# Kernel tuning notes

Measured on AMD Instinct MI355X. Metric: run time of the kernel, lower is better.

The kernel has to match this reference:

```python
import jax, jax.numpy as jnp
import numpy as np

B, T, D, H, E, O, A = 8192, 223, 7, 128, 50, 29, 9
IMPUTE_W, LABEL_W = 0.3, 1.0

def setup_inputs() -> dict:
    key = jax.random.key(0)
    ks = jax.random.split(key, 32)
    u = lambda k, shape, fan: jax.random.uniform(k, shape, jnp.float32, -1.0/np.sqrt(fan), 1.0/np.sqrt(fan))
    return {
        'values':    jax.random.normal(ks[0], (B, T, D), jnp.float32),
        'masks':     (jax.random.uniform(ks[1], (B, T, D)) < 0.8).astype(jnp.float32),
        'deltas':    jax.random.uniform(ks[2], (B, T, D), jnp.float32) * 5.0,
        'probs':     jax.nn.softmax(jax.random.normal(ks[3], (B, O), jnp.float32), axis=1),
        'ancillary': jax.random.normal(ks[4], (B, A), jnp.float32),
        'labels':    jax.random.randint(ks[5], (B,), 0, O, jnp.int32),
        'W_td_h': u(ks[6], (H, D), H),  'b_td_h': u(ks[7], (H,), H),
        'W_td_x': u(ks[8], (D, D), D),  'b_td_x': u(ks[9], (D,), D),
        'W_hist': u(ks[10], (D, H), H), 'b_hist': u(ks[11], (D,), H),
        'W_feat': u(ks[12], (D, D), D), 'b_feat': u(ks[13], (D,), D),
        'W_comb': u(ks[14], (D, 2*D), 2*D), 'b_comb': u(ks[15], (D,), 2*D),
        'W_ih': u(ks[16], (4*H, 2*D), H), 'W_hh': u(ks[17], (4*H, H), H),
        'b_ih': u(ks[18], (4*H,), H),     'b_hh': u(ks[19], (4*H,), H),
        'W_anc': u(ks[20], (E, A), A),    'b_anc': u(ks[21], (E,), A),
        'W_cat': u(ks[22], (H, H + E), H + E), 'b_cat': u(ks[23], (H,), H + E),
        'W_out': u(ks[24], (O, H), H),    'b_out': u(ks[25], (O,), H),
    }

def _rits_forward(values, masks, deltas, probs, ancillary,
                  W_td_h, b_td_h, W_td_x, b_td_x, W_hist, b_hist,
                  W_feat, b_feat, W_comb, b_comb, W_ih, W_hh, b_ih, b_hh,
                  W_anc, b_anc, W_cat, b_cat, W_out, b_out):
    Bn = values.shape[0]
    td_x_diag = jnp.diag(W_td_x)                     # diag=True decay uses only diagonal
    Wf = W_feat * (1.0 - jnp.eye(D, dtype=W_feat.dtype))

    def step(carry, xt):
        h, c, xl = carry
        x, m, d = xt                                  # each [B, D]
        gamma_h = jnp.exp(-jax.nn.relu(d @ W_td_h.T + b_td_h))   # [B, H]
        gamma_x = jnp.exp(-jax.nn.relu(d * td_x_diag + b_td_x))  # [B, D]
        h = h * gamma_h
        x_h = h @ W_hist.T + b_hist
        msum = jnp.sum(m) + 1e-5
        xl = xl + jnp.sum(jnp.abs(x - x_h) * m) / msum
        x_c = m * x + (1.0 - m) * x_h
        z_h = x_c @ Wf.T + b_feat
        xl = xl + jnp.sum(jnp.abs(x - z_h) * m) / msum
        alpha = jnp.concatenate([gamma_x, m], axis=1) @ W_comb.T + b_comb
        c_h = alpha * z_h + (1.0 - alpha) * x_h
        xl = xl + jnp.sum(jnp.abs(x - c_h) * m) / msum
        c_c = m * x + (1.0 - m) * c_h
        inputs = jnp.concatenate([c_c, m], axis=1)    # [B, 2D]
        gates = inputs @ W_ih.T + b_ih + h @ W_hh.T + b_hh  # [B, 4H]
        i, f, g, o = jnp.split(gates, 4, axis=1)
        c = jax.nn.sigmoid(f) * c + jax.nn.sigmoid(i) * jnp.tanh(g)
        h = jax.nn.sigmoid(o) * jnp.tanh(c)
        return (h, c, xl), c_c

    h0 = jnp.zeros((Bn, H), values.dtype)
    c0 = jnp.zeros((Bn, H), values.dtype)
    xs = (jnp.swapaxes(values, 0, 1), jnp.swapaxes(masks, 0, 1), jnp.swapaxes(deltas, 0, 1))
    (h, c, x_loss), imps = jax.lax.scan(step, (h0, c0, jnp.float32(0.0)), xs)
    imputations = jnp.swapaxes(imps, 0, 1)           # [B, T, D]

    x_loss = x_loss * IMPUTE_W
    anc = jax.nn.relu(ancillary @ W_anc.T + b_anc)
    h = jax.nn.relu(jnp.concatenate([h, anc], axis=1) @ W_cat.T + b_cat)
    y_h = jax.nn.softmax(h @ W_out.T + b_out, axis=1)
    y_loss = jnp.sum((y_h - probs) ** 2) / (Bn + 1e-5) * LABEL_W
    return x_loss, y_loss, x_loss + y_loss, y_h, imputations

def reference(values, masks, deltas, probs, ancillary, labels,
              W_td_h, b_td_h, W_td_x, b_td_x, W_hist, b_hist,
              W_feat, b_feat, W_comb, b_comb, W_ih, W_hh, b_ih, b_hh,
              W_anc, b_anc, W_cat, b_cat, W_out, b_out):
    x_loss, y_loss, loss, y_h, imputations = _rits_forward(
        values, masks, deltas, probs, ancillary,
        W_td_h, b_td_h, W_td_x, b_td_x, W_hist, b_hist,
        W_feat, b_feat, W_comb, b_comb, W_ih, W_hh, b_ih, b_hh,
        W_anc, b_anc, W_cat, b_cat, W_out, b_out)
    return (x_loss, y_loss, loss, y_h, imputations, labels)
```

## Files before the change

kernel.cpp:

```cpp
#include <hip/hip_runtime.h>
#include <math.h>

#define B_ 8192
#define T_ 223
#define D_ 7
#define H_ 128
#define G_ 512
#define E_ 50
#define O_ 29
#define A_ 9
#define TD_ (T_*D_)
#define NB 32
#define NTHR 512
#define MB 8

#define WS_MINV  0
#define WS_ACC   (WS_MINV + T_)
#define WS_WCATT (WS_ACC + 2)
#define WS_HFIN  (WS_WCATT + 178*H_)

#define OUT_YH  3
#define OUT_IMP (OUT_YH + B_*O_)
#define OUT_LAB (OUT_IMP + B_*T_*D_)

typedef __attribute__((ext_vector_type(8))) short short8;
typedef __attribute__((ext_vector_type(4))) float floatx4;
#define MFMA16(Av,Bv,Cv) __builtin_amdgcn_mfma_f32_16x16x32_bf16((Av),(Bv),(Cv),0,0,0)

__device__ __forceinline__ unsigned short f2bf(float f) {
    unsigned int u = __builtin_bit_cast(unsigned int, f);
    return (unsigned short)((u + 0x7FFFu + ((u >> 16) & 1u)) >> 16);
}
__device__ __forceinline__ float bf2f(unsigned short s) {
    unsigned int u = ((unsigned int)s) << 16;
    return __builtin_bit_cast(float, u);
}
__device__ __forceinline__ float rcp_(float x)  { return __builtin_amdgcn_rcpf(x); }
__device__ __forceinline__ float sigm(float x)  { return rcp_(1.f + __expf(-x)); }
__device__ __forceinline__ float tanh_(float x) { return 1.f - 2.f*rcp_(1.f + __expf(2.f*x)); }

__global__ void rits_prep(const float* __restrict__ W_cat, float* __restrict__ ws)
{
    int idx = blockIdx.x * 256 + threadIdx.x;
    if (idx < H_*178) {
        int j = idx / 178, k = idx - j*178;
        ws[WS_WCATT + k*H_ + j] = W_cat[idx];
    }
    if (idx < 2) ws[WS_ACC + idx] = 0.f;
}

__global__ void rits_msum(const float* __restrict__ masks, float* __restrict__ ws)
{
    const int t = blockIdx.x, tid = threadIdx.x;
    float s = 0.f;
    for (int i = tid; i < B_*D_; i += 256) {
        int b = i / D_, q = i - b*D_;
        s += masks[b*TD_ + t*D_ + q];
    }
    for (int off = 32; off > 0; off >>= 1) s += __shfl_down(s, off, 64);
    __shared__ float r[4];
    if ((tid & 63) == 0) r[tid >> 6] = s;
    __syncthreads();
    if (tid == 0) ws[WS_MINV + t] = 1.f / (r[0]+r[1]+r[2]+r[3] + 1e-5f);
}

__global__ __launch_bounds__(NTHR, 2) void rits_main(
    const float* __restrict__ values, const float* __restrict__ masks, const float* __restrict__ deltas,
    const float* __restrict__ W_td_h, const float* __restrict__ b_td_h,
    const float* __restrict__ W_td_x, const float* __restrict__ b_td_x,
    const float* __restrict__ W_hist, const float* __restrict__ b_hist,
    const float* __restrict__ W_feat, const float* __restrict__ b_feat,
    const float* __restrict__ W_comb, const float* __restrict__ b_comb,
    const float* __restrict__ W_ih, const float* __restrict__ W_hh,
    const float* __restrict__ b_ih, const float* __restrict__ b_hh,
    float* __restrict__ ws, float* __restrict__ out)
{
    __shared__ __attribute__((aligned(16))) unsigned short hbuf[NB*168];
    __shared__ __attribute__((aligned(16))) unsigned short dbuf[NB*72];
    __shared__ __attribute__((aligned(16))) unsigned short whis_lds[16*136];
    __shared__ float xs[NB*8], msh[NB*8], dsl[NB*8];
    __shared__ float xh_l[NB*8], xc_l[NB*8], gx_l[NB*8];
    __shared__ float bhist_l[8], tdx_l[8], btdx_l[8];
    __shared__ float impbuf[NB*16*7];
    __shared__ float red[8];

    const int tid  = threadIdx.x;
    const int b0   = blockIdx.x * NB;
    const int lane = tid & 63;
    const int w    = tid >> 6;
    const int quad = lane >> 4;
    const int l15  = lane & 15;

    for (int i = tid; i < NB*168; i += NTHR) hbuf[i] = 0;
    for (int i = tid; i < NB*72;  i += NTHR) dbuf[i] = 0;
    for (int i = tid; i < 16*136; i += NTHR) {
        int r = i / 136, c = i - r*136;
        whis_lds[i] = (r < 7 && c < 128) ? f2bf(W_hist[r*H_ + c]) : 0;
    }
    if (tid < 8) {
        bhist_l[tid] = (tid < 7) ? b_hist[tid] : 0.f;
        tdx_l[tid]   = (tid < 7) ? W_td_x[tid*D_ + tid] : 0.f;
        btdx_l[tid]  = (tid < 7) ? b_td_x[tid] : 0.f;
    }

    short8 whhf[4][4];
    short8 winf[4];
    short8 wtdf;
    float  biasg_r[4][4];
    float  btdh_r[4];
    {
        union UU { short8 v; unsigned short u[8]; } fr;
        #pragma unroll
        for (int c = 0; c < 4; ++c) {
            const int j = (c*8 + w)*16 + l15;
            #pragma unroll
            for (int s = 0; s < 4; ++s) {
                const float* p = W_hh + j*H_ + s*32 + quad*8;
                #pragma unroll
                for (int e = 0; e < 8; ++e) fr.u[e] = f2bf(p[e]);
                whhf[c][s] = fr.v;
            }
            #pragma unroll
            for (int e = 0; e < 8; ++e) {
                int k = quad*8 + e;
                fr.u[e] = (k < 14) ? f2bf(W_ih[j*14 + k]) : (unsigned short)0;
            }
            winf[c] = fr.v;
            #pragma unroll
            for (int r = 0; r < 4; ++r) {
                int jj = (c*8 + w)*16 + quad*4 + r;
                biasg_r[c][r] = b_ih[jj] + b_hh[jj];
            }
        }
        #pragma unroll
        for (int e = 0; e < 8; ++e) {
            int k = quad*8 + e;
            fr.u[e] = (k < 7) ? f2bf(W_td_h[(w*16 + l15)*D_ + k]) : (unsigned short)0;
        }
        wtdf = fr.v;
        #pragma unroll
        for (int r = 0; r < 4; ++r) btdh_r[r] = b_td_h[w*16 + quad*4 + r];
    }

    const bool ldr = (tid < NB*D_);
    const int  lb  = tid / D_, li = tid - (tid/D_)*D_;
    float wfr[7], wcr[14], bfr = 0.f, bcr = 0.f;
    if (ldr) {
        #pragma unroll
        for (int k = 0; k < 7; ++k)  wfr[k] = (k == li) ? 0.f : W_feat[li*D_ + k];
        #pragma unroll
        for (int k = 0; k < 14; ++k) wcr[k] = W_comb[li*14 + k];
        bfr = b_feat[li];  bcr = b_comb[li];
    }

    float c_st[2][4] = {{0,0,0,0},{0,0,0,0}};
    float lacc = 0.f;

    const long gbase = (long)(b0 + lb)*TD_ + li;
    float rx = 0.f, rm = 0.f, rd = 0.f;
    if (ldr) { rx = values[gbase]; rm = masks[gbase]; rd = deltas[gbase]; }

    const float* minv = ws + WS_MINV;

    for (int t = 0; t < T_; ++t) {
        if (ldr) { xs[lb*8+li] = rx; msh[lb*8+li] = rm; dsl[lb*8+li] = rd; }
        __syncthreads();
        if (ldr && t + 1 < T_) {
            const long g = gbase + (long)(t+1)*D_;
            rx = values[g]; rm = masks[g]; rd = deltas[g];
        }

        floatx4 acc[4][2];
        #pragma unroll
        for (int c = 0; c < 4; ++c)
            #pragma unroll
            for (int nt = 0; nt < 2; ++nt) {
                floatx4 a = { biasg_r[c][0], biasg_r[c][1], biasg_r[c][2], biasg_r[c][3] };
                acc[c][nt] = a;
            }
        floatx4 xh0 = {0,0,0,0}, xh1 = {0,0,0,0};
        #pragma unroll
        for (int s = 0; s < 4; ++s) {
            short8 hb0 = *(const short8*)&hbuf[l15*168       + s*32 + quad*8];
            short8 hb1 = *(const short8*)&hbuf[(16+l15)*168  + s*32 + quad*8];
            #pragma unroll
            for (int c = 0; c < 4; ++c) {
                acc[c][0] = MFMA16(whhf[c][s], hb0, acc[c][0]);
                acc[c][1] = MFMA16(whhf[c][s], hb1, acc[c][1]);
            }
            if (w == 7) {
                short8 wh = *(const short8*)&whis_lds[l15*136 + s*32 + quad*8];
                xh0 = MFMA16(wh, hb0, xh0);
                xh1 = MFMA16(wh, hb1, xh1);
            }
        }
        if (w == 7 && quad < 2) {
            #pragma unroll
            for (int nt = 0; nt < 2; ++nt) {
                const int b = nt*16 + l15;
                floatx4 xv = nt ? xh1 : xh0;
                #pragma unroll
                for (int r = 0; r < 4; ++r) {
                    const int i = quad*4 + r;
                    if (i < 7) {
                        float xhv = xv[r] + bhist_l[i];
                        float x = xs[b*8+i], m = msh[b*8+i], d = dsl[b*8+i];
                        xh_l[b*8+i] = xhv;
                        xc_l[b*8+i] = m*x + (1.f-m)*xhv;
                        gx_l[b*8+i] = __expf(-fmaxf(fmaf(d, tdx_l[i], btdx_l[i]), 0.f));
                    }
                }
            }
        }
        __syncthreads();

        if (ldr) {
            const int b = lb, i = li;
            const float invt = minv[t];
            const float x = xs[b*8+i], m = msh[b*8+i];
            float zh = bfr;
            #pragma unroll
            for (int k = 0; k < 7; ++k) zh = fmaf(wfr[k], xc_l[b*8+k], zh);
            float al = bcr;
            #pragma unroll
            for (int k = 0; k < 7; ++k) al = fmaf(wcr[k],   gx_l[b*8+k], al);
            #pragma unroll
            for (int k = 0; k < 7; ++k) al = fmaf(wcr[7+k], msh[b*8+k], al);
            const float xhv = xh_l[b*8+i];
            const float ch  = al*zh + (1.f-al)*xhv;
            const float cc  = m*x + (1.f-m)*ch;
            impbuf[(b*16 + (t & 15))*7 + i] = cc;
            hbuf[b*168 + 128 + i] = f2bf(cc);
            hbuf[b*168 + 135 + i] = f2bf(m);
            dbuf[b*72 + i] = f2bf(rd);
            lacc = fmaf((fabsf(x-xhv) + fabsf(x-zh) + fabsf(x-ch)) * m, invt, lacc);
        }
        __syncthreads();

        {
            short8 ib0 = *(const short8*)&hbuf[l15*168      + 128 + quad*8];
            short8 ib1 = *(const short8*)&hbuf[(16+l15)*168 + 128 + quad*8];
            #pragma unroll
            for (int c = 0; c < 4; ++c) {
                acc[c][0] = MFMA16(winf[c], ib0, acc[c][0]);
                acc[c][1] = MFMA16(winf[c], ib1, acc[c][1]);
            }
        }
        floatx4 g0 = {0,0,0,0}, g1 = {0,0,0,0};
        const bool dec = (t + 1 < T_);
        if (dec) {
            short8 df0 = *(const short8*)&dbuf[l15*72      + quad*8];
            short8 df1 = *(const short8*)&dbuf[(16+l15)*72 + quad*8];
            floatx4 z = {0,0,0,0};
            g0 = MFMA16(wtdf, df0, z);
            g1 = MFMA16(wtdf, df1, z);
        }
        #pragma unroll
        for (int nt = 0; nt < 2; ++nt) {
            const int b = nt*16 + l15;
            floatx4 gg = nt ? g1 : g0;
            #pragma unroll
            for (int r = 0; r < 4; ++r) {
                float ig = acc[0][nt][r], fg = acc[1][nt][r];
                float gv = acc[2][nt][r], og = acc[3][nt][r];
                float cn = sigm(fg)*c_st[nt][r] + sigm(ig)*tanh_(gv);
                c_st[nt][r] = cn;
                float hn = sigm(og)*tanh_(cn);
                if (dec) hn *= __expf(-fmaxf(gg[r] + btdh_r[r], 0.f));
                hbuf[b*168 + w*16 + quad*4 + r] = f2bf(hn);
            }
        }

        if ((t & 15) == 15 || t == T_ - 1) {
            const int t0 = t & ~15;
            const int b  = tid >> 4, c16 = tid & 15;
            if (t0 + c16 <= t) {
                float* gp = out + (size_t)OUT_IMP + (size_t)(b0+b)*TD_ + (size_t)(t0+c16)*D_;
                const float* lp = &impbuf[(b*16 + c16)*7];
                #pragma unroll
                for (int e = 0; e < 7; ++e) gp[e] = lp[e];
            }
        }
    }
    __syncthreads();

    for (int off = 32; off > 0; off >>= 1) lacc += __shfl_down(lacc, off, 64);
    if ((tid & 63) == 0) red[tid >> 6] = lacc;
    __syncthreads();
    if (tid == 0) {
        float s = 0.f;
        #pragma unroll
        for (int q = 0; q < 8; ++q) s += red[q];
        atomicAdd(&ws[WS_ACC], s);
    }
    for (int i = tid; i < NB*H_; i += NTHR) {
        int b = i >> 7, j = i & 127;
        ws[WS_HFIN + (size_t)(b0+b)*H_ + j] = bf2f(hbuf[b*168 + j]);
    }
}

__global__ __launch_bounds__(128) void rits_head(
    const float* __restrict__ probs, const float* __restrict__ ancillary, const int* __restrict__ labels,
    const float* __restrict__ W_anc, const float* __restrict__ b_anc,
    const float* __restrict__ b_cat,
    const float* __restrict__ W_out, const float* __restrict__ b_out,
    float* __restrict__ ws, float* __restrict__ out)
{
    __shared__ float hb[MB*H_];
    __shared__ float ancl[MB*52];
    __shared__ float hc[MB*H_];
    __shared__ float lg[MB*32];
    __shared__ float smx[MB], sinv[MB], ysum[MB];
    __shared__ float sq[MB*32];
    const int tid = threadIdx.x;
    const int bb0 = blockIdx.x * MB;

    for (int i = tid; i < MB*H_; i += 128) hb[i] = ws[WS_HFIN + (size_t)bb0*H_ + i];
    for (int i = tid; i < MB*E_; i += 128) {
        int b = i / E_, e = i - b*E_;
        float s = b_anc[e];
        #pragma unroll
        for (int a = 0; a < A_; ++a) s = fmaf(ancillary[(bb0+b)*A_ + a], W_anc[e*A_ + a], s);
        ancl[b*52+e] = fmaxf(s, 0.f);
    }
    __syncthreads();
    {
        const int j = tid;
        float s[MB];
        #pragma unroll
        for (int b = 0; b < MB; ++b) s[b] = b_cat[j];
        const float* wc = ws + WS_WCATT;
        for (int k = 0; k < H_; ++k) {
            float wv = wc[k*H_ + j];
            #pragma unroll
            for (int b = 0; b < MB; ++b) s[b] = fmaf(hb[b*H_+k], wv, s[b]);
        }
        for (int k = 0; k < E_; ++k) {
            float wv = wc[(H_+k)*H_ + j];
            #pragma unroll
            for (int b = 0; b < MB; ++b) s[b] = fmaf(ancl[b*52+k], wv, s[b]);
        }
        #pragma unroll
        for (int b = 0; b < MB; ++b) hc[b*H_+j] = fmaxf(s[b], 0.f);
    }
    __syncthreads();
    for (int i = tid; i < MB*O_; i += 128) {
        int b = i / O_, o = i - b*O_;
        float s = b_out[o];
        for (int k = 0; k < H_; ++k) s = fmaf(hc[b*H_+k], W_out[o*H_+k], s);
        lg[b*32+o] = s;
    }
    __syncthreads();
    if (tid < MB) {
        float mx = -1e30f;
        for (int o = 0; o < O_; ++o) mx = fmaxf(mx, lg[tid*32+o]);
        float se = 0.f;
        for (int o = 0; o < O_; ++o) se += __expf(lg[tid*32+o] - mx);
        smx[tid] = mx; sinv[tid] = 1.f / se;
    }
    __syncthreads();
    for (int i = tid; i < MB*O_; i += 128) {
        int b = i / O_, o = i - b*O_;
        float y = __expf(lg[b*32+o] - smx[b]) * sinv[b];
        out[OUT_YH + (size_t)(bb0+b)*O_ + o] = y;
        float d = y - probs[(size_t)(bb0+b)*O_ + o];
        sq[b*32+o] = d*d;
    }
    __syncthreads();
    if (tid < MB) {
        float s = 0.f;
        for (int o = 0; o < O_; ++o) s += sq[tid*32+o];
        ysum[tid] = s;
        out[OUT_LAB + bb0 + tid] = (float)labels[bb0 + tid];
    }
    __syncthreads();
    if (tid == 0) {
        float s = 0.f;
        #pragma unroll
        for (int b = 0; b < MB; ++b) s += ysum[b];
        atomicAdd(&ws[WS_ACC+1], s);
    }
}

__global__ void rits_fin(const float* __restrict__ ws, float* __restrict__ out)
{
    if (blockIdx.x == 0 && threadIdx.x == 0) {
        float xl = ws[WS_ACC] * 0.3f;
        float yl = ws[WS_ACC+1] * (1.0f / (8192.0f + 1e-5f));
        out[0] = xl; out[1] = yl; out[2] = xl + yl;
    }
}

extern "C" void kernel_launch(void* const* d_in, const int* in_sizes, int n_in,
                              void* d_out, int out_size, void* d_ws, size_t ws_size,
                              hipStream_t stream)
{
    const float* values = (const float*)d_in[0];
    const float* masks  = (const float*)d_in[1];
    const float* deltas = (const float*)d_in[2];
    const float* probs  = (const float*)d_in[3];
    const float* ancil  = (const float*)d_in[4];
    const int*   labels = (const int*)  d_in[5];
    const float* W_td_h = (const float*)d_in[6];
    const float* b_td_h = (const float*)d_in[7];
    const float* W_td_x = (const float*)d_in[8];
    const float* b_td_x = (const float*)d_in[9];
    const float* W_hist = (const float*)d_in[10];
    const float* b_hist = (const float*)d_in[11];
    const float* W_feat = (const float*)d_in[12];
    const float* b_feat = (const float*)d_in[13];
    const float* W_comb = (const float*)d_in[14];
    const float* b_comb = (const float*)d_in[15];
    const float* W_ih   = (const float*)d_in[16];
    const float* W_hh   = (const float*)d_in[17];
    const float* b_ih   = (const float*)d_in[18];
    const float* b_hh   = (const float*)d_in[19];
    const float* W_anc  = (const float*)d_in[20];
    const float* b_anc  = (const float*)d_in[21];
    const float* W_cat  = (const float*)d_in[22];
    const float* b_cat  = (const float*)d_in[23];
    const float* W_out  = (const float*)d_in[24];
    const float* b_out  = (const float*)d_in[25];
    float* ws  = (float*)d_ws;
    float* out = (float*)d_out;

    hipLaunchKernelGGL(rits_prep, dim3((H_*178 + 255)/256), dim3(256), 0, stream, W_cat, ws);
    hipLaunchKernelGGL(rits_msum, dim3(T_), dim3(256), 0, stream, masks, ws);
    hipLaunchKernelGGL(rits_main, dim3(B_/NB), dim3(NTHR), 0, stream,
                       values, masks, deltas, W_td_h, b_td_h, W_td_x, b_td_x,
                       W_hist, b_hist, W_feat, b_feat, W_comb, b_comb,
                       W_ih, W_hh, b_ih, b_hh, ws, out);
    hipLaunchKernelGGL(rits_head, dim3(B_/MB), dim3(128), 0, stream,
                       probs, ancil, labels, W_anc, b_anc, b_cat, W_out, b_out, ws, out);
    hipLaunchKernelGGL(rits_fin, dim3(1), dim3(1), 0, stream, ws, out);
}
```

Baseline: 1.041 ms.

## Halve batch per block, fuse mask-sum into main loop via per-step atomics

Each block now handles 16 batch rows instead of 32, which doubles the grid to 512 blocks and raises the occupancy bound to 4 blocks per CU, so more CUs share the serial recurrence. The separate mask-sum kernel is dropped: the main loop accumulates each step's loss term and mask count through per-timestep atomics, and the final kernel divides them. The W_ih columns are interleaved so cc and m can be packed into one 32-bit LDS store, and h is written as packed bf16. The trade-off is per-step atomics from every block and halved MFMA N-tile utilisation per wave.

```diff
diff --git a/kernel.cpp b/kernel.cpp
--- a/kernel.cpp
+++ b/kernel.cpp
@@ -1,4 +1,5 @@
 #include <hip/hip_runtime.h>
+#include <hip/hip_bf16.h>
 #include <math.h>
 
 #define B_ 8192
@@ -10,13 +11,13 @@
 #define O_ 29
 #define A_ 9
 #define TD_ (T_*D_)
-#define NB 32
+#define NB 16
 #define NTHR 512
 #define MB 8
 
-#define WS_MINV  0
-#define WS_ACC   (WS_MINV + T_)
-#define WS_WCATT (WS_ACC + 2)
+#define WS_TACC  0
+#define WS_ACC   (WS_TACC + 2*T_)
+#define WS_WCATT (WS_ACC + 1)
 #define WS_HFIN  (WS_WCATT + 178*H_)
 
 #define OUT_YH  3
@@ -28,8 +29,8 @@
 #define MFMA16(Av,Bv,Cv) __builtin_amdgcn_mfma_f32_16x16x32_bf16((Av),(Bv),(Cv),0,0,0)
 
 __device__ __forceinline__ unsigned short f2bf(float f) {
-    unsigned int u = __builtin_bit_cast(unsigned int, f);
-    return (unsigned short)((u + 0x7FFFu + ((u >> 16) & 1u)) >> 16);
+    __hip_bfloat16 h = __float2bfloat16(f);
+    return __builtin_bit_cast(unsigned short, h);
 }
 __device__ __forceinline__ float bf2f(unsigned short s) {
     unsigned int u = ((unsigned int)s) << 16;
@@ -46,25 +47,10 @@
         int j = idx / 178, k = idx - j*178;
         ws[WS_WCATT + k*H_ + j] = W_cat[idx];
     }
-    if (idx < 2) ws[WS_ACC + idx] = 0.f;
-}
-
-__global__ void rits_msum(const float* __restrict__ masks, float* __restrict__ ws)
-{
-    const int t = blockIdx.x, tid = threadIdx.x;
-    float s = 0.f;
-    for (int i = tid; i < B_*D_; i += 256) {
-        int b = i / D_, q = i - b*D_;
-        s += masks[b*TD_ + t*D_ + q];
-    }
-    for (int off = 32; off > 0; off >>= 1) s += __shfl_down(s, off, 64);
-    __shared__ float r[4];
-    if ((tid & 63) == 0) r[tid >> 6] = s;
-    __syncthreads();
-    if (tid == 0) ws[WS_MINV + t] = 1.f / (r[0]+r[1]+r[2]+r[3] + 1e-5f);
-}
-
-__global__ __launch_bounds__(NTHR, 2) void rits_main(
+    if (idx < 2*T_ + 1) ws[WS_TACC + idx] = 0.f;
+}
+
+__global__ __launch_bounds__(NTHR, 4) void rits_main(
     const float* __restrict__ values, const float* __restrict__ masks, const float* __restrict__ deltas,
     const float* __restrict__ W_td_h, const float* __restrict__ b_td_h,
     const float* __restrict__ W_td_x, const float* __restrict__ b_td_x,
@@ -82,7 +68,6 @@
     __shared__ float xh_l[NB*8], xc_l[NB*8], gx_l[NB*8];
     __shared__ float bhist_l[8], tdx_l[8], btdx_l[8];
     __shared__ float impbuf[NB*16*7];
-    __shared__ float red[8];
 
     const int tid  = threadIdx.x;
     const int b0   = blockIdx.x * NB;
@@ -123,7 +108,8 @@
             #pragma unroll
             for (int e = 0; e < 8; ++e) {
                 int k = quad*8 + e;
-                fr.u[e] = (k < 14) ? f2bf(W_ih[j*14 + k]) : (unsigned short)0;
+                fr.u[e] = (k < 14) ? f2bf(W_ih[j*14 + (k >> 1) + ((k & 1) ? 7 : 0)])
+                                   : (unsigned short)0;
             }
             winf[c] = fr.v;
             #pragma unroll
@@ -153,14 +139,11 @@
         bfr = b_feat[li];  bcr = b_comb[li];
     }
 
-    float c_st[2][4] = {{0,0,0,0},{0,0,0,0}};
-    float lacc = 0.f;
+    float c_st[4] = {0,0,0,0};
 
     const long gbase = (long)(b0 + lb)*TD_ + li;
     float rx = 0.f, rm = 0.f, rd = 0.f;
     if (ldr) { rx = values[gbase]; rm = masks[gbase]; rd = deltas[gbase]; }
-
-    const float* minv = ws + WS_MINV;
 
     for (int t = 0; t < T_; ++t) {
         if (ldr) { xs[lb*8+li] = rx; msh[lb*8+li] = rm; dsl[lb*8+li] = rd; }
@@ -170,53 +153,43 @@
             rx = values[g]; rm = masks[g]; rd = deltas[g];
         }
 
-        floatx4 acc[4][2];
-        #pragma unroll
-        for (int c = 0; c < 4; ++c)
-            #pragma unroll
-            for (int nt = 0; nt < 2; ++nt) {
-                floatx4 a = { biasg_r[c][0], biasg_r[c][1], biasg_r[c][2], biasg_r[c][3] };
-                acc[c][nt] = a;
-            }
-        floatx4 xh0 = {0,0,0,0}, xh1 = {0,0,0,0};
+        floatx4 acc[4];
+        #pragma unroll
+        for (int c = 0; c < 4; ++c) {
+            floatx4 a = { biasg_r[c][0], biasg_r[c][1], biasg_r[c][2], biasg_r[c][3] };
+            acc[c] = a;
+        }
+        floatx4 xh0 = {0,0,0,0};
         #pragma unroll
         for (int s = 0; s < 4; ++s) {
-            short8 hb0 = *(const short8*)&hbuf[l15*168       + s*32 + quad*8];
-            short8 hb1 = *(const short8*)&hbuf[(16+l15)*168  + s*32 + quad*8];
-            #pragma unroll
-            for (int c = 0; c < 4; ++c) {
-                acc[c][0] = MFMA16(whhf[c][s], hb0, acc[c][0]);
-                acc[c][1] = MFMA16(whhf[c][s], hb1, acc[c][1]);
-            }
+            short8 hb0 = *(const short8*)&hbuf[l15*168 + s*32 + quad*8];
+            #pragma unroll
+            for (int c = 0; c < 4; ++c)
+                acc[c] = MFMA16(whhf[c][s], hb0, acc[c]);
             if (w == 7) {
                 short8 wh = *(const short8*)&whis_lds[l15*136 + s*32 + quad*8];
                 xh0 = MFMA16(wh, hb0, xh0);
-                xh1 = MFMA16(wh, hb1, xh1);
             }
         }
         if (w == 7 && quad < 2) {
-            #pragma unroll
-            for (int nt = 0; nt < 2; ++nt) {
-                const int b = nt*16 + l15;
-                floatx4 xv = nt ? xh1 : xh0;
-                #pragma unroll
-                for (int r = 0; r < 4; ++r) {
-                    const int i = quad*4 + r;
-                    if (i < 7) {
-                        float xhv = xv[r] + bhist_l[i];
-                        float x = xs[b*8+i], m = msh[b*8+i], d = dsl[b*8+i];
-                        xh_l[b*8+i] = xhv;
-                        xc_l[b*8+i] = m*x + (1.f-m)*xhv;
-                        gx_l[b*8+i] = __expf(-fmaxf(fmaf(d, tdx_l[i], btdx_l[i]), 0.f));
-                    }
+            const int b = l15;
+            #pragma unroll
+            for (int r = 0; r < 4; ++r) {
+                const int i = quad*4 + r;
+                if (i < 7) {
+                    float xhv = xh0[r] + bhist_l[i];
+                    float x = xs[b*8+i], m = msh[b*8+i], d = dsl[b*8+i];
+                    xh_l[b*8+i] = xhv;
+                    xc_l[b*8+i] = m*x + (1.f-m)*xhv;
+                    gx_l[b*8+i] = __expf(-fmaxf(fmaf(d, tdx_l[i], btdx_l[i]), 0.f));
                 }
             }
         }
         __syncthreads();
 
+        float term = 0.f, msump = 0.f;
         if (ldr) {
             const int b = lb, i = li;
-            const float invt = minv[t];
             const float x = xs[b*8+i], m = msh[b*8+i];
             float zh = bfr;
             #pragma unroll
@@ -230,69 +203,72 @@
             const float ch  = al*zh + (1.f-al)*xhv;
             const float cc  = m*x + (1.f-m)*ch;
             impbuf[(b*16 + (t & 15))*7 + i] = cc;
-            hbuf[b*168 + 128 + i] = f2bf(cc);
-            hbuf[b*168 + 135 + i] = f2bf(m);
+            *(unsigned int*)&hbuf[b*168 + 128 + 2*i] =
+                (unsigned int)f2bf(cc) | ((unsigned int)f2bf(m) << 16);
             dbuf[b*72 + i] = f2bf(rd);
-            lacc = fmaf((fabsf(x-xhv) + fabsf(x-zh) + fabsf(x-ch)) * m, invt, lacc);
+            term  = (fabsf(x-xhv) + fabsf(x-zh) + fabsf(x-ch)) * m;
+            msump = m;
+        }
+        if (w < 2) {
+            #pragma unroll
+            for (int off = 32; off > 0; off >>= 1) {
+                term  += __shfl_down(term,  off, 64);
+                msump += __shfl_down(msump, off, 64);
+            }
+            if (lane == 0) {
+                atomicAdd(&ws[WS_TACC + 2*t    ], term);
+                atomicAdd(&ws[WS_TACC + 2*t + 1], msump);
+            }
         }
         __syncthreads();
 
         {
-            short8 ib0 = *(const short8*)&hbuf[l15*168      + 128 + quad*8];
-            short8 ib1 = *(const short8*)&hbuf[(16+l15)*168 + 128 + quad*8];
-            #pragma unroll
-            for (int c = 0; c < 4; ++c) {
-                acc[c][0] = MFMA16(winf[c], ib0, acc[c][0]);
-                acc[c][1] = MFMA16(winf[c], ib1, acc[c][1]);
-            }
-        }
-        floatx4 g0 = {0,0,0,0}, g1 = {0,0,0,0};
+            short8 ib0 = *(const short8*)&hbuf[l15*168 + 128 + quad*8];
+            #pragma unroll
+            for (int c = 0; c < 4; ++c)
+                acc[c] = MFMA16(winf[c], ib0, acc[c]);
+        }
+        floatx4 g0 = {0,0,0,0};
         const bool dec = (t + 1 < T_);
         if (dec) {
-            short8 df0 = *(const short8*)&dbuf[l15*72      + quad*8];
-            short8 df1 = *(const short8*)&dbuf[(16+l15)*72 + quad*8];
+            short8 df0 = *(const short8*)&dbuf[l15*72 + quad*8];
             floatx4 z = {0,0,0,0};
             g0 = MFMA16(wtdf, df0, z);
-            g1 = MFMA16(wtdf, df1, z);
-        }
-        #pragma unroll
-        for (int nt = 0; nt < 2; ++nt) {
-            const int b = nt*16 + l15;
-            floatx4 gg = nt ? g1 : g0;
+        }
+        {
+            const int b = l15;
+            float hv[4];
             #pragma unroll
             for (int r = 0; r < 4; ++r) {
-                float ig = acc[0][nt][r], fg = acc[1][nt][r];
-                float gv = acc[2][nt][r], og = acc[3][nt][r];
-                float cn = sigm(fg)*c_st[nt][r] + sigm(ig)*tanh_(gv);
-                c_st[nt][r] = cn;
+                float ig = acc[0][r], fg = acc[1][r];
+                float gv = acc[2][r], og = acc[3][r];
+                float cn = sigm(fg)*c_st[r] + sigm(ig)*tanh_(gv);
+                c_st[r] = cn;
                 float hn = sigm(og)*tanh_(cn);
-                if (dec) hn *= __expf(-fmaxf(gg[r] + btdh_r[r], 0.f));
-                hbuf[b*168 + w*16 + quad*4 + r] = f2bf(hn);
-            }
+                if (dec) hn *= __expf(-fmaxf(g0[r] + btdh_r[r], 0.f));
+                hv[r] = hn;
+            }
+            uint2 pk;
+            pk.x = (unsigned int)f2bf(hv[0]) | ((unsigned int)f2bf(hv[1]) << 16);
+            pk.y = (unsigned int)f2bf(hv[2]) | ((unsigned int)f2bf(hv[3]) << 16);
+            *(uint2*)&hbuf[b*168 + w*16 + quad*4] = pk;
         }
 
         if ((t & 15) == 15 || t == T_ - 1) {
             const int t0 = t & ~15;
-            const int b  = tid >> 4, c16 = tid & 15;
-            if (t0 + c16 <= t) {
-                float* gp = out + (size_t)OUT_IMP + (size_t)(b0+b)*TD_ + (size_t)(t0+c16)*D_;
-                const float* lp = &impbuf[(b*16 + c16)*7];
-                #pragma unroll
-                for (int e = 0; e < 7; ++e) gp[e] = lp[e];
-            }
-        }
-    }
-    __syncthreads();
-
-    for (int off = 32; off > 0; off >>= 1) lacc += __shfl_down(lacc, off, 64);
-    if ((tid & 63) == 0) red[tid >> 6] = lacc;
-    __syncthreads();
-    if (tid == 0) {
-        float s = 0.f;
-        #pragma unroll
-        for (int q = 0; q < 8; ++q) s += red[q];
-        atomicAdd(&ws[WS_ACC], s);
-    }
+            if (tid < 256) {
+                const int b = tid >> 4, c16 = tid & 15;
+                if (t0 + c16 <= t) {
+                    float* gp = out + (size_t)OUT_IMP + (size_t)(b0+b)*TD_ + (size_t)(t0+c16)*D_;
+                    const float* lp = &impbuf[(b*16 + c16)*7];
+                    #pragma unroll
+                    for (int e = 0; e < 7; ++e) gp[e] = lp[e];
+                }
+            }
+        }
+    }
+    __syncthreads();
+
     for (int i = tid; i < NB*H_; i += NTHR) {
         int b = i >> 7, j = i & 127;
         ws[WS_HFIN + (size_t)(b0+b)*H_ + j] = bf2f(hbuf[b*168 + j]);
@@ -378,15 +354,18 @@
         float s = 0.f;
         #pragma unroll
         for (int b = 0; b < MB; ++b) s += ysum[b];
-        atomicAdd(&ws[WS_ACC+1], s);
+        atomicAdd(&ws[WS_ACC], s);
     }
 }
 
 __global__ void rits_fin(const float* __restrict__ ws, float* __restrict__ out)
 {
     if (blockIdx.x == 0 && threadIdx.x == 0) {
-        float xl = ws[WS_ACC] * 0.3f;
-        float yl = ws[WS_ACC+1] * (1.0f / (8192.0f + 1e-5f));
+        float xl = 0.f;
+        for (int t = 0; t < T_; ++t)
+            xl += ws[WS_TACC + 2*t] / (ws[WS_TACC + 2*t + 1] + 1e-5f);
+        xl *= 0.3f;
+        float yl = ws[WS_ACC] * (1.0f / (8192.0f + 1e-5f));
         out[0] = xl; out[1] = yl; out[2] = xl + yl;
     }
 }
@@ -425,7 +404,6 @@
     float* out = (float*)d_out;
 
     hipLaunchKernelGGL(rits_prep, dim3((H_*178 + 255)/256), dim3(256), 0, stream, W_cat, ws);
-    hipLaunchKernelGGL(rits_msum, dim3(T_), dim3(256), 0, stream, masks, ws);
     hipLaunchKernelGGL(rits_main, dim3(B_/NB), dim3(NTHR), 0, stream,
                        values, masks, deltas, W_td_h, b_td_h, W_td_x, b_td_x,
                        W_hist, b_hist, W_feat, b_feat, W_comb, b_comb,
```

After: 3.627 ms. 248% more time.
